# Kernel optimization log

Measured on AMD Instinct MI355X. Metric: run time of the kernel, lower is better.

## Reference

```python
import jax, jax.numpy as jnp
import numpy as np

B, LQ, LK, DQ, DK, DV = 8, 2048, 2048, 1024, 1024, 1024
TOP_K = 64
NEG_INF = float('-inf')


def setup_inputs() -> dict:
    key = jax.random.key(0)
    kq, kk, kv, km, kw = jax.random.split(key, 5)
    queries = jax.random.normal(kq, (B, LQ, DQ), dtype=jnp.float32)
    keys = jax.random.normal(kk, (B, LK, DK), dtype=jnp.float32)
    values = jax.random.normal(kv, (B, LK, DV), dtype=jnp.float32)
    mask = jax.random.randint(km, (B, LQ, LK), 0, 2, dtype=jnp.int32)
    # nn.Linear(query_dim, key_dim, bias=False) weight: [key_dim, query_dim]
    W = jax.random.normal(kw, (DK, DQ), dtype=jnp.float32) / np.sqrt(DQ)
    return {"queries": queries, "keys": keys, "values": values,
            "mask": mask, "W": W, "top_k": TOP_K}


def reference(queries, keys, values, mask, W, top_k):
    # scores = (queries @ W.T) @ keys^T  -> [B, LQ, LK]  (method='general')
    q_proj = jnp.einsum('bqd,kd->bqk', queries, W)  # [B, LQ, DK]
    scores = jnp.einsum('bqd,btd->bqt', q_proj, keys)  # [B, LQ, LK]
    scores = jnp.where(mask == 0, NEG_INF, scores)
    alphas = jax.nn.softmax(scores, axis=-1)
    alphas = jnp.where(jnp.isnan(alphas), 0.0, alphas)  # fully-masked rows -> 0
    # top-k: zero out non-top-k probabilities, then re-softmax over the
    # resulting tensor (zeros contribute exp(0)=1, matching torch semantics)
    _, idx = jax.lax.top_k(alphas, top_k)  # [B, LQ, top_k]
    b_idx = jnp.arange(alphas.shape[0])[:, None, None]
    q_idx = jnp.arange(alphas.shape[1])[None, :, None]
    topk_mask = jnp.zeros(alphas.shape, alphas.dtype).at[b_idx, q_idx, idx].set(1.0)
    alphas = jnp.where(topk_mask == 0, 0.0, alphas)
    alphas = jax.nn.softmax(alphas, axis=-1)
    alphas = jnp.where(jnp.isnan(alphas), 0.0, alphas)
    # dropout_rate = 0.0 -> identity
    return jnp.einsum('bqt,btd->bqd', alphas, values)  # [B, LQ, DV]
```

## Files before the change

kernel.cpp:

```cpp
#include <hip/hip_runtime.h>
#include <math.h>

#define BATCH 8
#define SEQ   2048
#define DIM   1024
#define TOPK  64
#define NEGMASK -1e30f
#define CAND_THRESH 16.0f
#define CAP 28

typedef _Float16 f16;
typedef _Float16 f16x8 __attribute__((ext_vector_type(8)));
typedef float f32x4 __attribute__((ext_vector_type(4)));

__device__ __forceinline__ void async_load16(const void* g, void* l) {
  __builtin_amdgcn_global_load_lds(
      (const __attribute__((address_space(1))) void*)g,
      (__attribute__((address_space(3))) void*)l, 16, 0, 0);
}

__device__ __forceinline__ uint2 cvt4(float4 v) {
  union { f16 h[4]; uint2 u; } pk;
  pk.h[0] = (f16)v.x; pk.h[1] = (f16)v.y; pk.h[2] = (f16)v.z; pk.h[3] = (f16)v.w;
  return pk.u;
}

__global__ __launch_bounds__(256) void prep_kernel(
    const float* __restrict__ queries, const float* __restrict__ W,
    f16* __restrict__ q16, f16* __restrict__ w16) {
  const int blk = blockIdx.x;
  if (blk < 4096) {
    const float4* src = (const float4*)queries;
    uint2* dst = (uint2*)q16;
    const int base = blk * 1024 + threadIdx.x;
    float4 v0 = src[base];
    float4 v1 = src[base + 256];
    float4 v2 = src[base + 512];
    float4 v3 = src[base + 768];
    dst[base]       = cvt4(v0);
    dst[base + 256] = cvt4(v1);
    dst[base + 512] = cvt4(v2);
    dst[base + 768] = cvt4(v3);
  } else {
    const float4* src = (const float4*)W;
    uint2* dst = (uint2*)w16;
    const int base = (blk - 4096) * 1024 + threadIdx.x;
    float4 v0 = src[base];
    float4 v1 = src[base + 256];
    float4 v2 = src[base + 512];
    float4 v3 = src[base + 768];
    dst[base]       = cvt4(v0);
    dst[base + 256] = cvt4(v1);
    dst[base + 512] = cvt4(v2);
    dst[base + 768] = cvt4(v3);
  }
}


#define STAGEK(KOFF, BUF)                                                   \
  async_load16(srcA0 + (KOFF), smA + (BUF) * 8192 + wave * 2048);           \
  async_load16(srcA1 + (KOFF), smA + (BUF) * 8192 + wave * 2048 + 1024);    \
  async_load16(srcB0 + (KOFF), smB + (BUF) * 8192 + wave * 2048);           \
  async_load16(srcB1 + (KOFF), smB + (BUF) * 8192 + wave * 2048 + 1024);

#define GEMM_PROLOGUE(APTR, BPTR)                                           \
  const int tid = threadIdx.x;                                              \
  const int wave = tid >> 6, lane = tid & 63;                               \
  const int wm = (wave >> 1) * 64, wn = (wave & 1) * 64;                    \
  const int r0 = wave * 32 + (lane >> 2);                                   \
  const int c16 = (lane & 3) ^ ((r0 >> 1) & 3);                            \
  const f16* srcA0 = (APTR) + (size_t)(m0 + r0) * DIM + c16 * 8;           \
  const f16* srcA1 = (APTR) + (size_t)(m0 + r0 + 16) * DIM + c16 * 8;      \
  const f16* srcB0 = (BPTR) + (size_t)(n0 + r0) * DIM + c16 * 8;           \
  const f16* srcB1 = (BPTR) + (size_t)(n0 + r0 + 16) * DIM + c16 * 8;      \
  int offA[4], offB[4];                                                     \
  _Pragma("unroll")                                                         \
  for (int i = 0; i < 4; ++i) {                                             \
    int r = wm + i * 16 + (lane & 15);                                      \
    offA[i] = r * 64 + ((lane >> 4) ^ ((r >> 1) & 3)) * 16;                 \
    int rn = wn + i * 16 + (lane & 15);                                     \
    offB[i] = rn * 64 + ((lane >> 4) ^ ((rn >> 1) & 3)) * 16;               \
  }                                                                         \
  f32x4 acc[4][4];                                                          \
  _Pragma("unroll")                                                         \
  for (int i = 0; i < 4; ++i)                                               \
    _Pragma("unroll")                                                       \
    for (int j = 0; j < 4; ++j)                                             \
      acc[i][j] = (f32x4){0.f, 0.f, 0.f, 0.f};                              \
  STAGEK(0, 0)                                                              \
  STAGEK(32, 1)                                                             \
  int cur = 0;                                                              \
  for (int k0 = 0; k0 < DIM; k0 += 32) {                                    \
    if (k0 + 64 < DIM) {                                                    \
      const int nx2 = cur >= 1 ? cur - 1 : cur + 2;          \
      STAGEK(k0 + 64, nx2)                                                  \
      asm volatile("s_waitcnt vmcnt(8)" ::: "memory");                      \
    } else if (k0 + 32 < DIM) {                                             \
      asm volatile("s_waitcnt vmcnt(4)" ::: "memory");                      \
    } else {                                                                \
      asm volatile("s_waitcnt vmcnt(0)" ::: "memory");                      \
    }                                                                       \
    __builtin_amdgcn_s_barrier();                                           \
    asm volatile("" ::: "memory");                                          \
    f16x8 af[4], bf[4];                                                     \
    _Pragma("unroll")                                                       \
    for (int i = 0; i < 4; ++i) {                                           \
      af[i] = *(const f16x8*)(smA + cur * 8192 + offA[i]);                  \
      bf[i] = *(const f16x8*)(smB + cur * 8192 + offB[i]);                  \
    }                                                                       \
    _Pragma("unroll")                                                       \
    for (int i = 0; i < 4; ++i)                                             \
      _Pragma("unroll")                                                     \
      for (int j = 0; j < 4; ++j)                                           \
        acc[i][j] = __builtin_amdgcn_mfma_f32_16x16x32_f16(                 \
            af[i], bf[j], acc[i][j], 0, 0, 0);                              \
    asm volatile("" ::: "memory");                                          \
    __builtin_amdgcn_s_barrier();                                           \
    cur = cur == 2 ? 0 : cur + 1;                                           \
  }

__global__ __launch_bounds__(256, 3) void gemm_qproj(
    const f16* __restrict__ A, const f16* __restrict__ Bw,
    f16* __restrict__ C,
    const float* __restrict__ keys, f16* __restrict__ k16,
    const float* __restrict__ values, float* __restrict__ partial) {
  __shared__ __align__(128) char smA[24576];
  __shared__ __align__(128) char smB[24576];
  if (blockIdx.x >= 5120) {
    const int bid = (int)blockIdx.x - 5120;
    int tc = bid >> 5;
    int b  = (bid >> 2) & 7;
    int dg = bid & 3;
    int d  = dg * 256 + threadIdx.x;
    const float* vp = values + ((size_t)b * SEQ + (size_t)tc * 64) * DIM + d;
    float s = 0.f;
    #pragma unroll 8
    for (int t = 0; t < 64; ++t) s += vp[(size_t)t * DIM];
    partial[((size_t)tc * BATCH + b) * DIM + d] = s;
    return;
  }
  if (blockIdx.x >= 1024) {
    const float4* src = (const float4*)keys;
    uint2* dst = (uint2*)k16;
    const int base = ((int)blockIdx.x - 1024) * 1024 + threadIdx.x;
    float4 v0 = src[base];
    float4 v1 = src[base + 256];
    float4 v2 = src[base + 512];
    float4 v3 = src[base + 768];
    dst[base]       = cvt4(v0);
    dst[base + 256] = cvt4(v1);
    dst[base + 512] = cvt4(v2);
    dst[base + 768] = cvt4(v3);
    return;
  }
  const int swz = ((int)blockIdx.x & 7) * 128 + ((int)blockIdx.x >> 3);
  const int m0 = (swz >> 3) * 128;
  const int n0 = (swz & 7) * 128;
  GEMM_PROLOGUE(A, Bw)
  const int cr = m0 + wm + (lane >> 4) * 4;
  const int cc = n0 + wn + (lane & 15);
  #pragma unroll
  for (int i = 0; i < 4; ++i)
    #pragma unroll
    for (int j = 0; j < 4; ++j)
      #pragma unroll
      for (int reg = 0; reg < 4; ++reg)
        C[(size_t)(cr + i * 16 + reg) * DIM + cc + j * 16] = (f16)acc[i][j][reg];
}

__global__ __launch_bounds__(256, 3) void gemm_scores(
    const f16* __restrict__ QP, const f16* __restrict__ K16,
    const int* __restrict__ mask,
    float2* __restrict__ cand,
    int* __restrict__ counts,
    const float* __restrict__ partial, float* __restrict__ colsum) {
  __shared__ __align__(128) char smA[24576];
  __shared__ __align__(128) char smB[24576];
  if (blockIdx.x >= 2048) {
    int idx = ((int)blockIdx.x - 2048) * 256 + threadIdx.x;
    float s = 0.f;
    #pragma unroll
    for (int tc = 0; tc < 32; ++tc) s += partial[(size_t)tc * 8192 + idx];
    colsum[idx] = s;
    return;
  }
  const int swz = ((int)blockIdx.x & 7) * 256 + ((int)blockIdx.x >> 3);
  const int m0 = (swz >> 4) * 128;
  const int n0 = (swz & 15) * 128;
  const int b  = m0 >> 11;
  const f16* Bk = K16 + (size_t)b * SEQ * DIM;
  GEMM_PROLOGUE(QP, Bk)

  const int g  = lane >> 4;
  const int lc = lane & 15;

  #pragma unroll
  for (int i = 0; i < 4; ++i)
    #pragma unroll
    for (int reg = 0; reg < 4; ++reg) {
      const int r = wm + i * 16 + g * 4 + reg;
      const int* mp = mask + (size_t)(m0 + r) * SEQ + n0 + wn + lc;
      int m0v = mp[0], m1v = mp[16], m2v = mp[32], m3v = mp[48];
      if (m0v == 0) acc[i][0][reg] = NEGMASK;
      if (m1v == 0) acc[i][1][reg] = NEGMASK;
      if (m2v == 0) acc[i][2][reg] = NEGMASK;
      if (m3v == 0) acc[i][3][reg] = NEGMASK;
    }

  float* hm = (float*)smA;
  #pragma unroll
  for (int i = 0; i < 4; ++i)
    #pragma unroll
    for (int reg = 0; reg < 4; ++reg) {
      const int r = wm + i * 16 + g * 4 + reg;
      float m4 = fmaxf(fmaxf(acc[i][0][reg], acc[i][1][reg]),
                       fmaxf(acc[i][2][reg], acc[i][3][reg]));
      #pragma unroll
      for (int off = 8; off >= 1; off >>= 1) m4 = fmaxf(m4, __shfl_xor(m4, off));
      if (lc == 0) hm[r * 2 + (wn >> 6)] = m4;
    }
  __syncthreads();

  const int pairbase = (n0 >> 7) * 2 + (wn >> 6);
  #pragma unroll
  for (int i = 0; i < 4; ++i)
    #pragma unroll
    for (int reg = 0; reg < 4; ++reg) {
      const int r = wm + i * 16 + g * 4 + reg;
      const float tm = fmaxf(hm[r * 2], hm[r * 2 + 1]);
      const float thresh = fmaxf(tm - CAND_THRESH, -1e29f);
      float2* slot = cand + ((size_t)(m0 + r) * 32 + pairbase) * CAP;
      int cnt = 0;
      #pragma unroll
      for (int j = 0; j < 4; ++j) {
        const float s = acc[i][j][reg];
        const bool c = s > thresh;
        const unsigned long long bal = __ballot(c);
        const int seg = (int)((bal >> (g * 16)) & 0xFFFFull);
        const int pos = cnt + __popc(seg & ((1 << lc) - 1));
        if (c && pos < CAP) {
          float2 e; e.x = s; e.y = __int_as_float(n0 + wn + j * 16 + lc);
          slot[pos] = e;
        }
        cnt += __popc(seg);
      }
      if (lc == 0) counts[(size_t)(m0 + r) * 32 + pairbase] = cnt < CAP ? cnt : CAP;
    }
}

__global__ __launch_bounds__(512) void topk_kernel(
    const float2* __restrict__ cand,
    const int*    __restrict__ counts,
    const float*  __restrict__ values,
    const float*  __restrict__ colsum,
    float* __restrict__ out)
{
  __shared__ float ssc[8][128];
  __shared__ int   sidx[8][128];
  const int wave = threadIdx.x >> 6;
  const int lane = threadIdx.x & 63;
  const int grow = blockIdx.x * 8 + wave;
  const int b    = grow >> 11;
  float* msc = ssc[wave];
  int*   mix = sidx[wave];

  int cnt_p = 0;
  if (lane < 32) cnt_p = counts[(size_t)grow * 32 + lane];
  const float2* myslots = cand + ((size_t)grow * 32 + lane) * CAP;

  float mv = -3e38f;
  for (int k = 0; k < cnt_p; ++k) mv = fmaxf(mv, myslots[k].x);
  #pragma unroll
  for (int off = 32; off > 0; off >>= 1) mv = fmaxf(mv, __shfl_xor(mv, off));
  const bool dead = (mv <= -1e29f);

  float total_g = 0.f;
  f32x4 oacc[4];
  #pragma unroll
  for (int j = 0; j < 4; ++j) oacc[j] = (f32x4){0.f, 0.f, 0.f, 0.f};
  const float* vbase = values + (size_t)b * SEQ * DIM;

  if (!dead) {
    const float thresh = mv - CAND_THRESH;
    int f = 0; float zp = 0.f;
    for (int k = 0; k < cnt_p; ++k) {
      float s = myslots[k].x;
      if (s > thresh) { ++f; zp += __expf(s - mv); }
    }
    int incl = f;
    #pragma unroll
    for (int off = 1; off < 64; off <<= 1) {
      int t = __shfl_up(incl, off);
      if (lane >= off) incl += t;
    }
    const int base = incl - f;
    const int F = __shfl(incl, 63);
    #pragma unroll
    for (int off = 32; off > 0; off >>= 1) zp += __shfl_xor(zp, off);
    const float Z = zp;
    int w = 0;
    for (int k = 0; k < cnt_p; ++k) {
      float2 cv = myslots[k];
      if (cv.x > thresh) {
        int p = base + w;
        if (p < 128) { msc[p] = cv.x; mix[p] = __float_as_int(cv.y); }
        ++w;
      }
    }
    asm volatile("s_waitcnt lgkmcnt(0)" ::: "memory");

    if (F <= TOPK) {
      for (int c = 0; c < F; ++c) {
        float g = expm1f(__expf(msc[c] - mv) / Z);
        total_g += g;
        const float* vrow = vbase + (size_t)mix[c] * DIM;
        #pragma unroll
        for (int j = 0; j < 4; ++j) {
          f32x4 v = *(const f32x4*)(vrow + j * 256 + lane * 4);
          #pragma unroll
          for (int e = 0; e < 4; ++e) oacc[j][e] = fmaf(g, v[e], oacc[j][e]);
        }
      }
    } else {
      const int nlist = F < 128 ? F : 128;
      for (int itk = 0; itk < TOPK; ++itk) {
        float bv = -3e38f; int bi = 1 << 30; int bsl = -1;
        #pragma unroll
        for (int h = 0; h < 2; ++h) {
          int sl = lane + h * 64;
          if (sl < nlist) {
            float v = msc[sl]; int id = mix[sl];
            if (v > bv || (v == bv && id < bi)) { bv = v; bi = id; bsl = sl; }
          }
        }
        #pragma unroll
        for (int off = 32; off > 0; off >>= 1) {
          float ov = __shfl_xor(bv, off);
          int   oi = __shfl_xor(bi, off);
          int   os = __shfl_xor(bsl, off);
          if (ov > bv || (ov == bv && oi < bi)) { bv = ov; bi = oi; bsl = os; }
        }
        if (bv <= -1e29f) break;
        float g = expm1f(__expf(bv - mv) / Z);
        total_g += g;
        const float* vrow = vbase + (size_t)bi * DIM;
        #pragma unroll
        for (int j = 0; j < 4; ++j) {
          f32x4 v = *(const f32x4*)(vrow + j * 256 + lane * 4);
          #pragma unroll
          for (int e = 0; e < 4; ++e) oacc[j][e] = fmaf(g, v[e], oacc[j][e]);
        }
        if (lane == 0) msc[bsl] = -3e38f;
        asm volatile("s_waitcnt lgkmcnt(0)" ::: "memory");
      }
    }
  }

  const float inv = 1.0f / (2048.0f + total_g);
  const float* cs = colsum + (size_t)b * DIM;
  float* orow = out + (size_t)grow * DIM;
  #pragma unroll
  for (int j = 0; j < 4; ++j) {
    f32x4 c = *(const f32x4*)(cs + j * 256 + lane * 4);
    f32x4 o;
    #pragma unroll
    for (int e = 0; e < 4; ++e) o[e] = (c[e] + oacc[j][e]) * inv;
    *(f32x4*)(orow + j * 256 + lane * 4) = o;
  }
}

extern "C" void kernel_launch(void* const* d_in, const int* in_sizes, int n_in,
                              void* d_out, int out_size, void* d_ws, size_t ws_size,
                              hipStream_t stream) {
  const float* queries = (const float*)d_in[0];
  const float* keys    = (const float*)d_in[1];
  const float* values  = (const float*)d_in[2];
  const int*   mask    = (const int*)d_in[3];
  const float* W       = (const float*)d_in[4];
  float* out = (float*)d_out;

  char* base = (char*)d_ws;
  float2* cand   = (float2*)base;
  f16*   q16     = (f16*)base;
  f16*   w16     = (f16*)(base + (size_t)32 * 1024 * 1024);
  int*   counts  = (int*)(base + (size_t)112 * 1024 * 1024);
  float* colsum  = (float*)(base + (size_t)118 * 1024 * 1024);
  float* partial = (float*)(base + (size_t)119 * 1024 * 1024);
  f16*   qp16    = (f16*)(base + (size_t)128 * 1024 * 1024);
  f16*   k16     = (f16*)(base + (size_t)160 * 1024 * 1024);

  prep_kernel<<<4352, 256, 0, stream>>>(queries, W, q16, w16);
  gemm_qproj<<<6144, 256, 0, stream>>>(q16, w16, qp16, keys, k16, values, partial);
  gemm_scores<<<2080, 256, 0, stream>>>(qp16, k16, mask, cand, counts,
                                        partial, colsum);
  topk_kernel<<<2048, 512, 0, stream>>>(cand, counts, values, colsum, out);
}
```

Baseline: 274.5 us.

## Switch GEMM blocks to 512 threads with 16-row-per-wave warp tiling

Both GEMM kernels now use 8 waves per 128x128 tile, with each wave owning 16 rows by 128 columns (1 A fragment, 8 B fragments) instead of 4 waves each owning 64x64. Staging is split so each thread issues 2 async loads per k-step, and the side tasks (key conversion, value column sums, colsum reduction) are remapped to 512-thread blocks with adjusted grid sizes. The aim is more waves to hide latency and fewer accumulator registers per wave. The cost is lower per-wave operand reuse: B fragments are read from LDS 8 times per A fragment, which raises LDS traffic per MFMA. The score epilogue also drops the shared-memory cross-wave max, since one wave now spans the full 128-column tile.

```diff
diff --git a/kernel.cpp b/kernel.cpp
--- a/kernel.cpp
+++ b/kernel.cpp
@@ -58,35 +58,23 @@
 
 
 #define STAGEK(KOFF, BUF)                                                   \
-  async_load16(srcA0 + (KOFF), smA + (BUF) * 8192 + wave * 2048);           \
-  async_load16(srcA1 + (KOFF), smA + (BUF) * 8192 + wave * 2048 + 1024);    \
-  async_load16(srcB0 + (KOFF), smB + (BUF) * 8192 + wave * 2048);           \
-  async_load16(srcB1 + (KOFF), smB + (BUF) * 8192 + wave * 2048 + 1024);
+  async_load16(srcA0 + (KOFF), smA + (BUF) * 8192 + wave * 1024);           \
+  async_load16(srcB0 + (KOFF), smB + (BUF) * 8192 + wave * 1024);
 
 #define GEMM_PROLOGUE(APTR, BPTR)                                           \
   const int tid = threadIdx.x;                                              \
   const int wave = tid >> 6, lane = tid & 63;                               \
-  const int wm = (wave >> 1) * 64, wn = (wave & 1) * 64;                    \
-  const int r0 = wave * 32 + (lane >> 2);                                   \
-  const int c16 = (lane & 3) ^ ((r0 >> 1) & 3);                            \
-  const f16* srcA0 = (APTR) + (size_t)(m0 + r0) * DIM + c16 * 8;           \
-  const f16* srcA1 = (APTR) + (size_t)(m0 + r0 + 16) * DIM + c16 * 8;      \
-  const f16* srcB0 = (BPTR) + (size_t)(n0 + r0) * DIM + c16 * 8;           \
-  const f16* srcB1 = (BPTR) + (size_t)(n0 + r0 + 16) * DIM + c16 * 8;      \
-  int offA[4], offB[4];                                                     \
+  const int l15 = lane & 15;                                                \
+  const int r0 = wave * 16 + (lane >> 2);                                   \
+  const int c16 = (lane & 3) ^ ((r0 >> 1) & 3);                             \
+  const f16* srcA0 = (APTR) + (size_t)(m0 + r0) * DIM + c16 * 8;            \
+  const f16* srcB0 = (BPTR) + (size_t)(n0 + r0) * DIM + c16 * 8;            \
+  const int ra = wave * 16 + l15;                                           \
+  const int offA = ra * 64 + (((lane >> 4) ^ ((ra >> 1) & 3)) * 16);        \
+  const int offB0 = l15 * 64 + (((lane >> 4) ^ ((l15 >> 1) & 3)) * 16);     \
+  f32x4 acc[8];                                                             \
   _Pragma("unroll")                                                         \
-  for (int i = 0; i < 4; ++i) {                                             \
-    int r = wm + i * 16 + (lane & 15);                                      \
-    offA[i] = r * 64 + ((lane >> 4) ^ ((r >> 1) & 3)) * 16;                 \
-    int rn = wn + i * 16 + (lane & 15);                                     \
-    offB[i] = rn * 64 + ((lane >> 4) ^ ((rn >> 1) & 3)) * 16;               \
-  }                                                                         \
-  f32x4 acc[4][4];                                                          \
-  _Pragma("unroll")                                                         \
-  for (int i = 0; i < 4; ++i)                                               \
-    _Pragma("unroll")                                                       \
-    for (int j = 0; j < 4; ++j)                                             \
-      acc[i][j] = (f32x4){0.f, 0.f, 0.f, 0.f};                              \
+  for (int fn = 0; fn < 8; ++fn) acc[fn] = (f32x4){0.f, 0.f, 0.f, 0.f};     \
   STAGEK(0, 0)                                                              \
   STAGEK(32, 1)                                                             \
   int cur = 0;                                                              \
@@ -94,44 +82,41 @@
     if (k0 + 64 < DIM) {                                                    \
       const int nx2 = cur >= 1 ? cur - 1 : cur + 2;          \
       STAGEK(k0 + 64, nx2)                                                  \
-      asm volatile("s_waitcnt vmcnt(8)" ::: "memory");                      \
+      asm volatile("s_waitcnt vmcnt(4)" ::: "memory");                      \
     } else if (k0 + 32 < DIM) {                                             \
-      asm volatile("s_waitcnt vmcnt(4)" ::: "memory");                      \
+      asm volatile("s_waitcnt vmcnt(2)" ::: "memory");                      \
     } else {                                                                \
       asm volatile("s_waitcnt vmcnt(0)" ::: "memory");                      \
     }                                                                       \
     __builtin_amdgcn_s_barrier();                                           \
     asm volatile("" ::: "memory");                                          \
-    f16x8 af[4], bf[4];                                                     \
+    f16x8 af = *(const f16x8*)(smA + cur * 8192 + offA);                    \
+    f16x8 bf[8];                                                            \
     _Pragma("unroll")                                                       \
-    for (int i = 0; i < 4; ++i) {                                           \
-      af[i] = *(const f16x8*)(smA + cur * 8192 + offA[i]);                  \
-      bf[i] = *(const f16x8*)(smB + cur * 8192 + offB[i]);                  \
-    }                                                                       \
+    for (int fn = 0; fn < 8; ++fn)                                          \
+      bf[fn] = *(const f16x8*)(smB + cur * 8192 + fn * 1024 + offB0);       \
     _Pragma("unroll")                                                       \
-    for (int i = 0; i < 4; ++i)                                             \
-      _Pragma("unroll")                                                     \
-      for (int j = 0; j < 4; ++j)                                           \
-        acc[i][j] = __builtin_amdgcn_mfma_f32_16x16x32_f16(                 \
-            af[i], bf[j], acc[i][j], 0, 0, 0);                              \
+    for (int fn = 0; fn < 8; ++fn)                                          \
+      acc[fn] = __builtin_amdgcn_mfma_f32_16x16x32_f16(                     \
+          af, bf[fn], acc[fn], 0, 0, 0);                                    \
     asm volatile("" ::: "memory");                                          \
     __builtin_amdgcn_s_barrier();                                           \
     cur = cur == 2 ? 0 : cur + 1;                                           \
   }
 
-__global__ __launch_bounds__(256, 3) void gemm_qproj(
+__global__ __launch_bounds__(512, 4) void gemm_qproj(
     const f16* __restrict__ A, const f16* __restrict__ Bw,
     f16* __restrict__ C,
     const float* __restrict__ keys, f16* __restrict__ k16,
     const float* __restrict__ values, float* __restrict__ partial) {
   __shared__ __align__(128) char smA[24576];
   __shared__ __align__(128) char smB[24576];
-  if (blockIdx.x >= 5120) {
-    const int bid = (int)blockIdx.x - 5120;
-    int tc = bid >> 5;
-    int b  = (bid >> 2) & 7;
-    int dg = bid & 3;
-    int d  = dg * 256 + threadIdx.x;
+  if (blockIdx.x >= 3072) {
+    const int bid = (int)blockIdx.x - 3072;
+    int tc = bid >> 4;
+    int b  = (bid >> 1) & 7;
+    int dg = bid & 1;
+    int d  = dg * 512 + threadIdx.x;
     const float* vp = values + ((size_t)b * SEQ + (size_t)tc * 64) * DIM + d;
     float s = 0.f;
     #pragma unroll 8
@@ -142,33 +127,32 @@
   if (blockIdx.x >= 1024) {
     const float4* src = (const float4*)keys;
     uint2* dst = (uint2*)k16;
-    const int base = ((int)blockIdx.x - 1024) * 1024 + threadIdx.x;
+    const int base = ((int)blockIdx.x - 1024) * 2048 + threadIdx.x;
     float4 v0 = src[base];
-    float4 v1 = src[base + 256];
-    float4 v2 = src[base + 512];
-    float4 v3 = src[base + 768];
-    dst[base]       = cvt4(v0);
-    dst[base + 256] = cvt4(v1);
-    dst[base + 512] = cvt4(v2);
-    dst[base + 768] = cvt4(v3);
+    float4 v1 = src[base + 512];
+    float4 v2 = src[base + 1024];
+    float4 v3 = src[base + 1536];
+    dst[base]        = cvt4(v0);
+    dst[base + 512]  = cvt4(v1);
+    dst[base + 1024] = cvt4(v2);
+    dst[base + 1536] = cvt4(v3);
     return;
   }
   const int swz = ((int)blockIdx.x & 7) * 128 + ((int)blockIdx.x >> 3);
   const int m0 = (swz >> 3) * 128;
   const int n0 = (swz & 7) * 128;
   GEMM_PROLOGUE(A, Bw)
-  const int cr = m0 + wm + (lane >> 4) * 4;
-  const int cc = n0 + wn + (lane & 15);
-  #pragma unroll
-  for (int i = 0; i < 4; ++i)
-    #pragma unroll
-    for (int j = 0; j < 4; ++j)
-      #pragma unroll
-      for (int reg = 0; reg < 4; ++reg)
-        C[(size_t)(cr + i * 16 + reg) * DIM + cc + j * 16] = (f16)acc[i][j][reg];
-}
-
-__global__ __launch_bounds__(256, 3) void gemm_scores(
+  const int g = lane >> 4;
+  #pragma unroll
+  for (int reg = 0; reg < 4; ++reg) {
+    const int cr = m0 + wave * 16 + g * 4 + reg;
+    #pragma unroll
+    for (int fn = 0; fn < 8; ++fn)
+      C[(size_t)cr * DIM + n0 + fn * 16 + l15] = (f16)acc[fn][reg];
+  }
+}
+
+__global__ __launch_bounds__(512, 4) void gemm_scores(
     const f16* __restrict__ QP, const f16* __restrict__ K16,
     const int* __restrict__ mask,
     float2* __restrict__ cand,
@@ -177,7 +161,7 @@
   __shared__ __align__(128) char smA[24576];
   __shared__ __align__(128) char smB[24576];
   if (blockIdx.x >= 2048) {
-    int idx = ((int)blockIdx.x - 2048) * 256 + threadIdx.x;
+    int idx = ((int)blockIdx.x - 2048) * 512 + threadIdx.x;
     float s = 0.f;
     #pragma unroll
     for (int tc = 0; tc < 32; ++tc) s += partial[(size_t)tc * 8192 + idx];
@@ -191,61 +175,43 @@
   const f16* Bk = K16 + (size_t)b * SEQ * DIM;
   GEMM_PROLOGUE(QP, Bk)
 
-  const int g  = lane >> 4;
-  const int lc = lane & 15;
-
-  #pragma unroll
-  for (int i = 0; i < 4; ++i)
-    #pragma unroll
-    for (int reg = 0; reg < 4; ++reg) {
-      const int r = wm + i * 16 + g * 4 + reg;
-      const int* mp = mask + (size_t)(m0 + r) * SEQ + n0 + wn + lc;
-      int m0v = mp[0], m1v = mp[16], m2v = mp[32], m3v = mp[48];
-      if (m0v == 0) acc[i][0][reg] = NEGMASK;
-      if (m1v == 0) acc[i][1][reg] = NEGMASK;
-      if (m2v == 0) acc[i][2][reg] = NEGMASK;
-      if (m3v == 0) acc[i][3][reg] = NEGMASK;
-    }
-
-  float* hm = (float*)smA;
-  #pragma unroll
-  for (int i = 0; i < 4; ++i)
-    #pragma unroll
-    for (int reg = 0; reg < 4; ++reg) {
-      const int r = wm + i * 16 + g * 4 + reg;
-      float m4 = fmaxf(fmaxf(acc[i][0][reg], acc[i][1][reg]),
-                       fmaxf(acc[i][2][reg], acc[i][3][reg]));
-      #pragma unroll
-      for (int off = 8; off >= 1; off >>= 1) m4 = fmaxf(m4, __shfl_xor(m4, off));
-      if (lc == 0) hm[r * 2 + (wn >> 6)] = m4;
-    }
-  __syncthreads();
-
-  const int pairbase = (n0 >> 7) * 2 + (wn >> 6);
-  #pragma unroll
-  for (int i = 0; i < 4; ++i)
-    #pragma unroll
-    for (int reg = 0; reg < 4; ++reg) {
-      const int r = wm + i * 16 + g * 4 + reg;
-      const float tm = fmaxf(hm[r * 2], hm[r * 2 + 1]);
-      const float thresh = fmaxf(tm - CAND_THRESH, -1e29f);
-      float2* slot = cand + ((size_t)(m0 + r) * 32 + pairbase) * CAP;
+  const int g = lane >> 4;
+  #pragma unroll
+  for (int reg = 0; reg < 4; ++reg) {
+    const int rloc = wave * 16 + g * 4 + reg;
+    const size_t grow = (size_t)m0 + rloc;
+    const int* mp = mask + grow * SEQ + n0 + l15;
+    #pragma unroll
+    for (int fn = 0; fn < 8; ++fn)
+      if (mp[fn * 16] == 0) acc[fn][reg] = NEGMASK;
+    float m8 = acc[0][reg];
+    #pragma unroll
+    for (int fn = 1; fn < 8; ++fn) m8 = fmaxf(m8, acc[fn][reg]);
+    #pragma unroll
+    for (int off = 8; off >= 1; off >>= 1) m8 = fmaxf(m8, __shfl_xor(m8, off));
+    const float thresh = fmaxf(m8 - CAND_THRESH, -1e29f);
+    #pragma unroll
+    for (int p = 0; p < 2; ++p) {
+      const int pairb = (n0 >> 6) + p;
+      float2* slot = cand + (grow * 32 + pairb) * CAP;
       int cnt = 0;
       #pragma unroll
       for (int j = 0; j < 4; ++j) {
-        const float s = acc[i][j][reg];
+        const float s = acc[p * 4 + j][reg];
         const bool c = s > thresh;
         const unsigned long long bal = __ballot(c);
         const int seg = (int)((bal >> (g * 16)) & 0xFFFFull);
-        const int pos = cnt + __popc(seg & ((1 << lc) - 1));
+        const int pos = cnt + __popc(seg & ((1 << l15) - 1));
         if (c && pos < CAP) {
-          float2 e; e.x = s; e.y = __int_as_float(n0 + wn + j * 16 + lc);
+          float2 e; e.x = s;
+          e.y = __int_as_float(n0 + p * 64 + j * 16 + l15);
           slot[pos] = e;
         }
         cnt += __popc(seg);
       }
-      if (lc == 0) counts[(size_t)(m0 + r) * 32 + pairbase] = cnt < CAP ? cnt : CAP;
-    }
+      if (l15 == 0) counts[grow * 32 + pairb] = cnt < CAP ? cnt : CAP;
+    }
+  }
 }
 
 __global__ __launch_bounds__(512) void topk_kernel(
@@ -390,8 +356,8 @@
   f16*   k16     = (f16*)(base + (size_t)160 * 1024 * 1024);
 
   prep_kernel<<<4352, 256, 0, stream>>>(queries, W, q16, w16);
-  gemm_qproj<<<6144, 256, 0, stream>>>(q16, w16, qp16, keys, k16, values, partial);
-  gemm_scores<<<2080, 256, 0, stream>>>(qp16, k16, mask, cand, counts,
+  gemm_qproj<<<3584, 512, 0, stream>>>(q16, w16, qp16, keys, k16, values, partial);
+  gemm_scores<<<2064, 512, 0, stream>>>(qp16, k16, mask, cand, counts,
                                         partial, colsum);
   topk_kernel<<<2048, 512, 0, stream>>>(cand, counts, values, colsum, out);
 }
```

After: 281.3 us. 2.5% more time.
